# Performance work log

Measured on AMD Instinct MI355X. Metric: run time of the kernel, lower is better.

## Reference

```python
import jax, jax.numpy as jnp
import numpy as np

N_NODES = 100000
N_EDGES = 3200000
N_GRAPHS = 512
HID = 64
OUT = 10


def setup_inputs() -> dict:
    key = jax.random.key(0)
    ks = jax.random.split(key, 10)
    x = jax.random.normal(ks[0], (N_NODES,), dtype=jnp.float32)
    edge_index = jax.random.randint(ks[1], (2, N_EDGES), 0, N_NODES, dtype=jnp.int64)
    batch = jnp.sort(jax.random.randint(ks[2], (N_NODES,), 0, N_GRAPHS, dtype=jnp.int64))
    # GCNConv weights (glorot) and zero biases, Linear layer params
    W1 = jax.random.normal(ks[3], (1, HID), dtype=jnp.float32) * (1.0 / np.sqrt(1 + HID))
    b1 = jnp.zeros((HID,), dtype=jnp.float32)
    W2 = jax.random.normal(ks[4], (HID, HID), dtype=jnp.float32) * (1.0 / np.sqrt(2 * HID))
    b2 = jnp.zeros((HID,), dtype=jnp.float32)
    Wl = jax.random.normal(ks[5], (2 * HID, OUT), dtype=jnp.float32) * (1.0 / np.sqrt(2 * HID))
    bl = jnp.zeros((OUT,), dtype=jnp.float32)
    return {"x": x, "edge_index": edge_index, "batch": batch,
            "W1": W1, "b1": b1, "W2": W2, "b2": b2, "Wl": Wl, "bl": bl}


def reference(x, edge_index, batch, W1, b1, W2, b2, Wl, bl):
    N = x.shape[0]
    loop = jnp.arange(N, dtype=edge_index.dtype)
    src = jnp.concatenate([edge_index[0], loop])  # add self-loops
    dst = jnp.concatenate([edge_index[1], loop])
    # symmetric GCN normalization: D^{-1/2} A_hat D^{-1/2}
    deg = jax.ops.segment_sum(jnp.ones_like(dst, dtype=jnp.float32), dst, num_segments=N)
    dinv = jax.lax.rsqrt(jnp.maximum(deg, 1.0))
    norm = (dinv[src] * dinv[dst])[:, None]  # [E+N, 1]

    def gcn(h, W, b):
        m = (h @ W)[src] * norm  # transform then gather messages
        return jax.ops.segment_sum(m, dst, num_segments=N) + b

    h0 = x[:, None]  # [N, 1] (dropout is identity at eval)
    x1 = jax.nn.relu(gcn(h0, W1, b1))
    x2 = jax.nn.relu(gcn(x1, W2, b2))
    xj = jnp.concatenate([x1, x2], axis=-1)  # JK 'cat' -> [N, 128]
    # global mean pool per graph
    cnt = jax.ops.segment_sum(jnp.ones((N,), jnp.float32), batch, num_segments=N_GRAPHS)
    pooled = jax.ops.segment_sum(xj, batch, num_segments=N_GRAPHS) / jnp.maximum(cnt, 1.0)[:, None]
    return pooled @ Wl + bl  # [G, 10]
```

## Files before the change

### kernel.cpp

```cpp
#include <hip/hip_runtime.h>
#include <hip/hip_bf16.h>

#define N_NODES 100000
#define N_EDGES 3200000
#define N_GRAPHS 512
#define HID 64
#define OUT_DIM 10

#define NPB 64
#define NB  1563
#define CAP 2432

__global__ __launch_bounds__(256) void k_part(const int4* __restrict__ src4,
                                              const int4* __restrict__ dst4,
                                              unsigned* __restrict__ bcur,
                                              unsigned* __restrict__ ebuf) {
    __shared__ unsigned hist[NB];
    __shared__ unsigned curs[NB];
    int tid = threadIdx.x;
    for (int i = tid; i < NB; i += 256) hist[i] = 0;
    __syncthreads();
    int4 s[2], d[2];
    int base4 = (blockIdx.x * 256 + tid) * 2;
    #pragma unroll
    for (int k = 0; k < 2; k++) {
        int i4 = base4 + k;
        if (i4 < N_EDGES / 4) { s[k] = src4[i4]; d[k] = dst4[i4]; }
        else { s[k] = make_int4(-1, -1, -1, -1); d[k] = make_int4(0, 0, 0, 0); }
    }
    #pragma unroll
    for (int k = 0; k < 2; k++) {
        if (s[k].x >= 0) {
            atomicAdd(&hist[d[k].x >> 6], 1u);
            atomicAdd(&hist[d[k].y >> 6], 1u);
            atomicAdd(&hist[d[k].z >> 6], 1u);
            atomicAdd(&hist[d[k].w >> 6], 1u);
        }
    }
    __syncthreads();
    for (int b = tid; b < NB; b += 256) {
        unsigned c = hist[b];
        curs[b] = c ? atomicAdd(&bcur[b], c) : 0u;
    }
    __syncthreads();
    #pragma unroll
    for (int k = 0; k < 2; k++) {
        if (s[k].x >= 0) {
            int ss[4] = { s[k].x, s[k].y, s[k].z, s[k].w };
            int dd[4] = { d[k].x, d[k].y, d[k].z, d[k].w };
            #pragma unroll
            for (int m = 0; m < 4; m++) {
                int b = dd[m] >> 6;
                unsigned dl = (unsigned)(dd[m] & 63);
                unsigned slot = atomicAdd(&curs[b], 1u);
                ebuf[(size_t)b * CAP + slot] = (dl << 24) | (unsigned)ss[m];
            }
        }
    }
}

__global__ __launch_bounds__(256) void k_buck1(const unsigned* __restrict__ ebuf,
                                               const unsigned* __restrict__ bcur,
                                               const float* __restrict__ x,
                                               unsigned* __restrict__ deg,
                                               float* __restrict__ dinv,
                                               float* __restrict__ g1) {
    __shared__ unsigned cnt[NPB];
    int b = blockIdx.x, tid = threadIdx.x;
    if (tid < NPB) cnt[tid] = 0;
    __syncthreads();
    int ec = (int)bcur[b];
    const unsigned* eb = ebuf + (size_t)b * CAP;
    for (int i = tid; i < ec; i += 256)
        atomicAdd(&cnt[eb[i] >> 24], 1u);
    __syncthreads();
    int n0 = b * NPB;
    int nn = min(NPB, N_NODES - n0);
    if (tid < nn) {
        unsigned c = cnt[tid];
        float dn = 1.0f / sqrtf((float)c + 1.0f);
        deg[n0 + tid] = c;
        dinv[n0 + tid] = dn;
        g1[n0 + tid] = dn * x[n0 + tid];
    }
}

__global__ __launch_bounds__(256) void k_buck2(const unsigned* __restrict__ ebuf,
                                               const unsigned* __restrict__ bcur,
                                               const float* __restrict__ g1,
                                               const float* __restrict__ dinv,
                                               const float* __restrict__ x,
                                               float2* __restrict__ sd) {
    __shared__ float sacc[NPB];
    int b = blockIdx.x, tid = threadIdx.x;
    if (tid < NPB) sacc[tid] = 0.f;
    __syncthreads();
    int ec = (int)bcur[b];
    const unsigned* eb = ebuf + (size_t)b * CAP;
    for (int i = tid; i < ec; i += 256) {
        unsigned w = eb[i];
        atomicAdd(&sacc[w >> 24], g1[w & 0x00FFFFFFu]);
    }
    __syncthreads();
    int n0 = b * NPB;
    int nn = min(NPB, N_NODES - n0);
    if (tid < nn) {
        float dn = dinv[n0 + tid];
        float s = dn * (sacc[tid] + dn * x[n0 + tid]);
        sd[n0 + tid] = make_float2(s, dn);
    }
}

__global__ __launch_bounds__(256, 4) void k_buck3(const unsigned* __restrict__ ebuf,
                                                  const unsigned* __restrict__ bcur,
                                                  const unsigned* __restrict__ deg,
                                                  const float2* __restrict__ sd,
                                                  const int* __restrict__ batch,
                                                  const float* __restrict__ W1,
                                                  const float* __restrict__ b1,
                                                  const float* __restrict__ W2,
                                                  const float* __restrict__ b2,
                                                  float* __restrict__ pooled) {
    __shared__ unsigned sorted[CAP];
    __shared__ float2 stage[256];
    __shared__ int offs[NPB + 1];
    __shared__ unsigned curs[NPB];
    int b = blockIdx.x, tid = threadIdx.x;
    int lane = tid & 63, wv = tid >> 6;
    int n0 = b * NPB;
    int nn = min(NPB, N_NODES - n0);
    if (tid == 0) {
        int r = 0;
        for (int i = 0; i < nn; i++) { offs[i] = r; curs[i] = (unsigned)r; r += (int)deg[n0 + i]; }
        offs[nn] = r;
    }
    float w2col[HID];
    #pragma unroll
    for (int j = 0; j < HID; j++) w2col[j] = W2[j * HID + lane];
    float w1 = W1[lane], bb1 = b1[lane], bb2 = b2[lane];
    __syncthreads();
    int ec = (int)bcur[b];
    const unsigned* eb = ebuf + (size_t)b * CAP;
    for (int i = tid; i < ec; i += 256) {
        unsigned w = eb[i];
        unsigned slot = atomicAdd(&curs[w >> 24], 1u);
        sorted[slot] = w;
    }
    __syncthreads();
    float2* st = stage + wv * 64;
    const float4* stv = (const float4*)st;
    int curg = -1;
    float pacc1 = 0.f, pacc2 = 0.f;

    auto fetchv = [&](int n) -> float2 {
        float2 v = make_float2(0.f, 0.f);
        if (n < nn) {
            int lo = offs[n];
            int m = offs[n + 1] - lo; if (m > 64) m = 64;
            if (lane < m) v = sd[sorted[lo + lane] & 0x00FFFFFFu];
        }
        return v;
    };

    float2 vcur = fetchv(wv);
    for (int n = wv; n < nn; n += 4) {
        float2 vnext = fetchv(n + 4);
        int lo = offs[n], hi = offs[n + 1];
        int m = hi - lo; if (m > 64) m = 64;
        st[lane] = vcur;
        float acca = 0.f, accb = 0.f;
        int k = 0;
        for (; k + 1 < m; k += 2) {
            float4 e = stv[k >> 1];
            acca = fmaf(e.y, fmaxf(fmaf(e.x, w1, bb1), 0.f), acca);
            accb = fmaf(e.w, fmaxf(fmaf(e.z, w1, bb1), 0.f), accb);
        }
        if (k < m) {
            float2 e0 = st[k];
            acca = fmaf(e0.y, fmaxf(fmaf(e0.x, w1, bb1), 0.f), acca);
        }
        for (int base = lo + 64; base < hi; base += 64) {
            int mm = hi - base; if (mm > 64) mm = 64;
            float2 v = make_float2(0.f, 0.f);
            if (lane < mm) v = sd[sorted[base + lane] & 0x00FFFFFFu];
            st[lane] = v;
            int kk = 0;
            for (; kk + 1 < mm; kk += 2) {
                float4 e = stv[kk >> 1];
                acca = fmaf(e.y, fmaxf(fmaf(e.x, w1, bb1), 0.f), acca);
                accb = fmaf(e.w, fmaxf(fmaf(e.z, w1, bb1), 0.f), accb);
            }
            if (kk < mm) {
                float2 e0 = st[kk];
                acca = fmaf(e0.y, fmaxf(fmaf(e0.x, w1, bb1), 0.f), acca);
            }
        }
        float2 self = sd[n0 + n];
        float t = fmaxf(fmaf(self.x, w1, bb1), 0.f);
        float a = self.y * (acca + accb + self.y * t);
        float acc2a = bb2, acc2b = 0.f;
        #pragma unroll
        for (int j = 0; j < HID; j += 2) {
            float aj0 = __int_as_float(__builtin_amdgcn_readlane(__float_as_int(a), j));
            float aj1 = __int_as_float(__builtin_amdgcn_readlane(__float_as_int(a), j + 1));
            acc2a = fmaf(aj0, w2col[j], acc2a);
            acc2b = fmaf(aj1, w2col[j + 1], acc2b);
        }
        float x2v = fmaxf(acc2a + acc2b, 0.f);
        int g = batch[n0 + n];
        if (g != curg) {
            if (curg >= 0) {
                atomicAdd(&pooled[curg * 2 * HID + lane], pacc1);
                atomicAdd(&pooled[curg * 2 * HID + HID + lane], pacc2);
            }
            curg = g; pacc1 = 0.f; pacc2 = 0.f;
        }
        pacc1 += t;
        pacc2 += x2v;
        vcur = vnext;
    }
    if (curg >= 0) {
        atomicAdd(&pooled[curg * 2 * HID + lane], pacc1);
        atomicAdd(&pooled[curg * 2 * HID + HID + lane], pacc2);
    }
}

__global__ __launch_bounds__(128) void k_head(const float* __restrict__ pooled,
                                              const int* __restrict__ batch,
                                              const float* __restrict__ Wl,
                                              const float* __restrict__ bl,
                                              float* __restrict__ out) {
    int g = blockIdx.x;
    int t = threadIdx.x;
    int lo1 = 0, hi1 = N_NODES;
    while (lo1 < hi1) { int mid = (lo1 + hi1) >> 1; if (batch[mid] < g) lo1 = mid + 1; else hi1 = mid; }
    int lo2 = lo1, hi2 = N_NODES;
    while (lo2 < hi2) { int mid = (lo2 + hi2) >> 1; if (batch[mid] < g + 1) lo2 = mid + 1; else hi2 = mid; }
    float denom = fmaxf((float)(lo2 - lo1), 1.f);
    __shared__ float pl[2 * HID];
    pl[t] = pooled[g * 2 * HID + t] / denom;
    __syncthreads();
    if (t < OUT_DIM) {
        float r = bl[t];
        #pragma unroll 16
        for (int j = 0; j < 2 * HID; j++) r = fmaf(pl[j], Wl[j * OUT_DIM + t], r);
        out[g * OUT_DIM + t] = r;
    }
}

extern "C" void kernel_launch(void* const* d_in, const int* in_sizes, int n_in,
                              void* d_out, int out_size, void* d_ws, size_t ws_size,
                              hipStream_t stream) {
    const float* x      = (const float*)d_in[0];
    const int*   ei     = (const int*)d_in[1];
    const int*   batch  = (const int*)d_in[2];
    const float* W1     = (const float*)d_in[3];
    const float* b1     = (const float*)d_in[4];
    const float* W2     = (const float*)d_in[5];
    const float* b2     = (const float*)d_in[6];
    const float* Wl     = (const float*)d_in[7];
    const float* bl     = (const float*)d_in[8];
    float* out = (float*)d_out;

    const int* src = ei;
    const int* dst = ei + N_EDGES;

    char* p = (char*)d_ws;
    auto alloc = [&](size_t bytes) { void* r = (void*)p; p += (bytes + 255) & ~(size_t)255; return r; };
    unsigned* bcur   = (unsigned*)alloc(NB * 4);
    unsigned* ebuf   = (unsigned*)alloc((size_t)NB * CAP * 4);
    unsigned* deg    = (unsigned*)alloc(N_NODES * 4);
    float*    dinv   = (float*)alloc(N_NODES * 4);
    float*    g1     = (float*)alloc(N_NODES * 4);
    float2*   sd     = (float2*)alloc((size_t)N_NODES * 8);
    float*    pooled = (float*)alloc((size_t)N_GRAPHS * 2 * HID * 4);

    hipMemsetAsync(bcur, 0, NB * 4, stream);
    hipMemsetAsync(pooled, 0, (size_t)N_GRAPHS * 2 * HID * 4, stream);

    const int TB = 256;
    int pbl = (N_EDGES / 8 + TB - 1) / TB;

    k_part <<<pbl, TB, 0, stream>>>((const int4*)src, (const int4*)dst, bcur, ebuf);
    k_buck1<<<NB, TB, 0, stream>>>(ebuf, bcur, x, deg, dinv, g1);
    k_buck2<<<NB, TB, 0, stream>>>(ebuf, bcur, g1, dinv, x, sd);
    k_buck3<<<NB, TB, 0, stream>>>(ebuf, bcur, deg, sd, batch, W1, b1, W2, b2, pooled);
    k_head <<<N_GRAPHS, 128, 0, stream>>>(pooled, batch, Wl, bl, out);
}
```

Before: 268.9 us.

## Sort bucket edges by destination once in buck1 and reuse in later passes

k_part now records each edge's shared-memory histogram rank during the counting pass, so the second pass of per-bucket shared atomics is gone and the second cursor array is freed. k_buck1 keeps per-edge ranks within each destination, computes offsets, and writes a destination-sorted copy of each bucket into a new ebuf2 buffer. k_buck2 and k_buck3 read that sorted copy, so k_buck3 no longer re-sorts into shared memory. k_buck3 also moves W2 from 64 per-lane registers into LDS to relieve register pressure, which adds an extra global buffer write and read and LDS reads inside the inner matvec loop.

```diff
diff --git a/kernel.cpp b/kernel.cpp
--- a/kernel.cpp
+++ b/kernel.cpp
@@ -16,45 +16,33 @@
                                               unsigned* __restrict__ bcur,
                                               unsigned* __restrict__ ebuf) {
     __shared__ unsigned hist[NB];
-    __shared__ unsigned curs[NB];
     int tid = threadIdx.x;
     for (int i = tid; i < NB; i += 256) hist[i] = 0;
     __syncthreads();
-    int4 s[2], d[2];
     int base4 = (blockIdx.x * 256 + tid) * 2;
+    int4 s0 = make_int4(-1, -1, -1, -1), s1 = s0;
+    int4 d0 = make_int4(0, 0, 0, 0), d1 = d0;
+    if (base4 < N_EDGES / 4)     { s0 = src4[base4];     d0 = dst4[base4]; }
+    if (base4 + 1 < N_EDGES / 4) { s1 = src4[base4 + 1]; d1 = dst4[base4 + 1]; }
+    int sv[8] = { s0.x, s0.y, s0.z, s0.w, s1.x, s1.y, s1.z, s1.w };
+    int dv[8] = { d0.x, d0.y, d0.z, d0.w, d1.x, d1.y, d1.z, d1.w };
+    int bk[8]; unsigned rk[8];
     #pragma unroll
-    for (int k = 0; k < 2; k++) {
-        int i4 = base4 + k;
-        if (i4 < N_EDGES / 4) { s[k] = src4[i4]; d[k] = dst4[i4]; }
-        else { s[k] = make_int4(-1, -1, -1, -1); d[k] = make_int4(0, 0, 0, 0); }
-    }
+    for (int k = 0; k < 8; k++) {
+        bk[k] = dv[k] >> 6;
+        rk[k] = (sv[k] >= 0) ? atomicAdd(&hist[bk[k]], 1u) : 0u;
+    }
+    __syncthreads();
+    for (int i = tid; i < NB; i += 256) {
+        unsigned c = hist[i];
+        hist[i] = c ? atomicAdd(&bcur[i], c) : 0u;
+    }
+    __syncthreads();
     #pragma unroll
-    for (int k = 0; k < 2; k++) {
-        if (s[k].x >= 0) {
-            atomicAdd(&hist[d[k].x >> 6], 1u);
-            atomicAdd(&hist[d[k].y >> 6], 1u);
-            atomicAdd(&hist[d[k].z >> 6], 1u);
-            atomicAdd(&hist[d[k].w >> 6], 1u);
-        }
-    }
-    __syncthreads();
-    for (int b = tid; b < NB; b += 256) {
-        unsigned c = hist[b];
-        curs[b] = c ? atomicAdd(&bcur[b], c) : 0u;
-    }
-    __syncthreads();
-    #pragma unroll
-    for (int k = 0; k < 2; k++) {
-        if (s[k].x >= 0) {
-            int ss[4] = { s[k].x, s[k].y, s[k].z, s[k].w };
-            int dd[4] = { d[k].x, d[k].y, d[k].z, d[k].w };
-            #pragma unroll
-            for (int m = 0; m < 4; m++) {
-                int b = dd[m] >> 6;
-                unsigned dl = (unsigned)(dd[m] & 63);
-                unsigned slot = atomicAdd(&curs[b], 1u);
-                ebuf[(size_t)b * CAP + slot] = (dl << 24) | (unsigned)ss[m];
-            }
+    for (int k = 0; k < 8; k++) {
+        if (sv[k] >= 0) {
+            unsigned dl = (unsigned)(dv[k] & 63);
+            ebuf[(size_t)bk[k] * CAP + hist[bk[k]] + rk[k]] = (dl << 24) | (unsigned)sv[k];
         }
     }
 }
@@ -64,15 +52,24 @@
                                                const float* __restrict__ x,
                                                unsigned* __restrict__ deg,
                                                float* __restrict__ dinv,
-                                               float* __restrict__ g1) {
+                                               float* __restrict__ g1,
+                                               unsigned* __restrict__ ebuf2) {
     __shared__ unsigned cnt[NPB];
+    __shared__ int offs[NPB];
+    __shared__ unsigned rnk[CAP];
     int b = blockIdx.x, tid = threadIdx.x;
     if (tid < NPB) cnt[tid] = 0;
     __syncthreads();
     int ec = (int)bcur[b];
     const unsigned* eb = ebuf + (size_t)b * CAP;
+    unsigned* eb2 = ebuf2 + (size_t)b * CAP;
     for (int i = tid; i < ec; i += 256)
-        atomicAdd(&cnt[eb[i] >> 24], 1u);
+        rnk[i] = atomicAdd(&cnt[eb[i] >> 24], 1u);
+    __syncthreads();
+    if (tid == 0) {
+        int r = 0;
+        for (int i = 0; i < NPB; i++) { offs[i] = r; r += (int)cnt[i]; }
+    }
     __syncthreads();
     int n0 = b * NPB;
     int nn = min(NPB, N_NODES - n0);
@@ -83,9 +80,13 @@
         dinv[n0 + tid] = dn;
         g1[n0 + tid] = dn * x[n0 + tid];
     }
-}
-
-__global__ __launch_bounds__(256) void k_buck2(const unsigned* __restrict__ ebuf,
+    for (int i = tid; i < ec; i += 256) {
+        unsigned w = eb[i];
+        eb2[offs[w >> 24] + rnk[i]] = w;
+    }
+}
+
+__global__ __launch_bounds__(256) void k_buck2(const unsigned* __restrict__ ebuf2,
                                                const unsigned* __restrict__ bcur,
                                                const float* __restrict__ g1,
                                                const float* __restrict__ dinv,
@@ -96,7 +97,7 @@
     if (tid < NPB) sacc[tid] = 0.f;
     __syncthreads();
     int ec = (int)bcur[b];
-    const unsigned* eb = ebuf + (size_t)b * CAP;
+    const unsigned* eb = ebuf2 + (size_t)b * CAP;
     for (int i = tid; i < ec; i += 256) {
         unsigned w = eb[i];
         atomicAdd(&sacc[w >> 24], g1[w & 0x00FFFFFFu]);
@@ -111,42 +112,32 @@
     }
 }
 
-__global__ __launch_bounds__(256, 4) void k_buck3(const unsigned* __restrict__ ebuf,
-                                                  const unsigned* __restrict__ bcur,
-                                                  const unsigned* __restrict__ deg,
-                                                  const float2* __restrict__ sd,
-                                                  const int* __restrict__ batch,
-                                                  const float* __restrict__ W1,
-                                                  const float* __restrict__ b1,
-                                                  const float* __restrict__ W2,
-                                                  const float* __restrict__ b2,
-                                                  float* __restrict__ pooled) {
-    __shared__ unsigned sorted[CAP];
+__global__ __launch_bounds__(256) void k_buck3(const unsigned* __restrict__ ebuf2,
+                                               const unsigned* __restrict__ bcur,
+                                               const unsigned* __restrict__ deg,
+                                               const float2* __restrict__ sd,
+                                               const int* __restrict__ batch,
+                                               const float* __restrict__ W1,
+                                               const float* __restrict__ b1,
+                                               const float* __restrict__ W2,
+                                               const float* __restrict__ b2,
+                                               float* __restrict__ pooled) {
+    __shared__ float w2ls[HID * HID];
     __shared__ float2 stage[256];
     __shared__ int offs[NPB + 1];
-    __shared__ unsigned curs[NPB];
     int b = blockIdx.x, tid = threadIdx.x;
     int lane = tid & 63, wv = tid >> 6;
     int n0 = b * NPB;
     int nn = min(NPB, N_NODES - n0);
     if (tid == 0) {
         int r = 0;
-        for (int i = 0; i < nn; i++) { offs[i] = r; curs[i] = (unsigned)r; r += (int)deg[n0 + i]; }
+        for (int i = 0; i < nn; i++) { offs[i] = r; r += (int)deg[n0 + i]; }
         offs[nn] = r;
     }
-    float w2col[HID];
-    #pragma unroll
-    for (int j = 0; j < HID; j++) w2col[j] = W2[j * HID + lane];
+    for (int i = tid; i < HID * HID; i += 256) w2ls[i] = W2[i];
     float w1 = W1[lane], bb1 = b1[lane], bb2 = b2[lane];
     __syncthreads();
-    int ec = (int)bcur[b];
-    const unsigned* eb = ebuf + (size_t)b * CAP;
-    for (int i = tid; i < ec; i += 256) {
-        unsigned w = eb[i];
-        unsigned slot = atomicAdd(&curs[w >> 24], 1u);
-        sorted[slot] = w;
-    }
-    __syncthreads();
+    const unsigned* eb2 = ebuf2 + (size_t)b * CAP;
     float2* st = stage + wv * 64;
     const float4* stv = (const float4*)st;
     int curg = -1;
@@ -157,7 +148,7 @@
         if (n < nn) {
             int lo = offs[n];
             int m = offs[n + 1] - lo; if (m > 64) m = 64;
-            if (lane < m) v = sd[sorted[lo + lane] & 0x00FFFFFFu];
+            if (lane < m) v = sd[eb2[lo + lane] & 0x00FFFFFFu];
         }
         return v;
     };
@@ -182,7 +173,7 @@
         for (int base = lo + 64; base < hi; base += 64) {
             int mm = hi - base; if (mm > 64) mm = 64;
             float2 v = make_float2(0.f, 0.f);
-            if (lane < mm) v = sd[sorted[base + lane] & 0x00FFFFFFu];
+            if (lane < mm) v = sd[eb2[base + lane] & 0x00FFFFFFu];
             st[lane] = v;
             int kk = 0;
             for (; kk + 1 < mm; kk += 2) {
@@ -203,8 +194,8 @@
         for (int j = 0; j < HID; j += 2) {
             float aj0 = __int_as_float(__builtin_amdgcn_readlane(__float_as_int(a), j));
             float aj1 = __int_as_float(__builtin_amdgcn_readlane(__float_as_int(a), j + 1));
-            acc2a = fmaf(aj0, w2col[j], acc2a);
-            acc2b = fmaf(aj1, w2col[j + 1], acc2b);
+            acc2a = fmaf(aj0, w2ls[j * HID + lane], acc2a);
+            acc2b = fmaf(aj1, w2ls[(j + 1) * HID + lane], acc2b);
         }
         float x2v = fmaxf(acc2a + acc2b, 0.f);
         int g = batch[n0 + n];
@@ -269,6 +260,7 @@
     auto alloc = [&](size_t bytes) { void* r = (void*)p; p += (bytes + 255) & ~(size_t)255; return r; };
     unsigned* bcur   = (unsigned*)alloc(NB * 4);
     unsigned* ebuf   = (unsigned*)alloc((size_t)NB * CAP * 4);
+    unsigned* ebuf2  = (unsigned*)alloc((size_t)NB * CAP * 4);
     unsigned* deg    = (unsigned*)alloc(N_NODES * 4);
     float*    dinv   = (float*)alloc(N_NODES * 4);
     float*    g1     = (float*)alloc(N_NODES * 4);
@@ -282,8 +274,8 @@
     int pbl = (N_EDGES / 8 + TB - 1) / TB;
 
     k_part <<<pbl, TB, 0, stream>>>((const int4*)src, (const int4*)dst, bcur, ebuf);
-    k_buck1<<<NB, TB, 0, stream>>>(ebuf, bcur, x, deg, dinv, g1);
-    k_buck2<<<NB, TB, 0, stream>>>(ebuf, bcur, g1, dinv, x, sd);
-    k_buck3<<<NB, TB, 0, stream>>>(ebuf, bcur, deg, sd, batch, W1, b1, W2, b2, pooled);
+    k_buck1<<<NB, TB, 0, stream>>>(ebuf, bcur, x, deg, dinv, g1, ebuf2);
+    k_buck2<<<NB, TB, 0, stream>>>(ebuf2, bcur, g1, dinv, x, sd);
+    k_buck3<<<NB, TB, 0, stream>>>(ebuf2, bcur, deg, sd, batch, W1, b1, W2, b2, pooled);
     k_head <<<N_GRAPHS, 128, 0, stream>>>(pooled, batch, Wl, bl, out);
 }
```

New measurement: 291.3 us. 8.3% more time.
